# Kernel tuning notes

Hardware: AMD Instinct MI355X
Metric: run time of the kernel (lower is better)

The kernel has to match this reference:

```python
import jax, jax.numpy as jnp
import numpy as np
import math

H_HEADS = 16
D_PER = 64
D_MODEL = 1024
B, L = 8, 1024


def _dual_attention(q1, k1, q2, k2, v):
    # all [B,h,L,d]; scores = avg of two scaled QK^T
    scale = 1.0 / math.sqrt(q1.shape[-1])
    s1 = jnp.einsum('bhqd,bhkd->bhqk', q1, k1) * scale
    s2 = jnp.einsum('bhqd,bhkd->bhqk', q2, k2) * scale
    p = jax.nn.softmax((s1 + s2) * 0.5, axis=-1)
    return jnp.einsum('bhqk,bhkd->bhqd', p, v)


def _proj(X, W, b):
    # [B,L,D] -> [B,h,L,d]
    Bb, Ll, _ = X.shape
    y = X @ W + b
    return y.reshape(Bb, Ll, H_HEADS, D_PER).transpose(0, 2, 1, 3)


def _mha(Q1, K1, Q2, K2, V, Wq, bq, Wk, bk, Wv, bv, Wo, bo):
    q1 = _proj(Q1, Wq, bq)
    k1 = _proj(K1, Wk, bk)
    q2 = _proj(Q2, Wq, bq)  # same linear as q1 (linears[0])
    k2 = _proj(K2, Wk, bk)  # same linear as k1 (linears[1])
    v = _proj(V, Wv, bv)
    o = _dual_attention(q1, k1, q2, k2, v)  # [B,h,L,d]
    Bb = o.shape[0]
    o = o.transpose(0, 2, 1, 3).reshape(Bb, -1, H_HEADS * D_PER)
    return o @ Wo + bo  # [B,L,D]


def setup_inputs() -> dict:
    key = jax.random.key(0)
    ks = jax.random.split(key, 5)
    sc = 1.0 / math.sqrt(D_MODEL)
    return {
        'x': jax.random.normal(ks[0], (B, L, 3, D_MODEL), jnp.float32),
        'Wq': jax.random.normal(ks[1], (D_MODEL, H_HEADS * D_PER), jnp.float32) * sc,
        'bq': jnp.zeros((H_HEADS * D_PER,), jnp.float32),
        'Wk': jax.random.normal(ks[2], (D_MODEL, H_HEADS * D_PER), jnp.float32) * sc,
        'bk': jnp.zeros((H_HEADS * D_PER,), jnp.float32),
        'Wv': jax.random.normal(ks[3], (D_MODEL, H_HEADS * D_PER), jnp.float32) * sc,
        'bv': jnp.zeros((H_HEADS * D_PER,), jnp.float32),
        'Wo': jax.random.normal(ks[4], (H_HEADS * D_PER, D_MODEL), jnp.float32) * sc,
        'bo': jnp.zeros((D_MODEL,), jnp.float32),
    }


def reference(x, Wq, bq, Wk, bk, Wv, bv, Wo, bo):
    Hx = x[:, :, 0, :]
    Tx = x[:, :, 1, :]
    Rx = x[:, :, 2, :]
    p = (Wq, bq, Wk, bk, Wv, bv, Wo, bo)
    H_new = _mha(Tx, Tx, Rx, Rx, Hx, *p)
    T_new = _mha(Hx, Hx, Rx, Rx, Tx, *p)
    R_new = _mha(Hx, Hx, Tx, Tx, Rx, *p)
    return jnp.stack([H_new, T_new, R_new], axis=2)  # [B,L,3,D]
```

## Files before the change

### kernel.cpp

```cpp
#include <hip/hip_runtime.h>
#include <hip/hip_bf16.h>
#include <stdint.h>

#define NTOK 8192
#define DM   1024

typedef __bf16 bf16x8 __attribute__((ext_vector_type(8)));
typedef float  f32x4  __attribute__((ext_vector_type(4)));

__device__ __forceinline__ unsigned short f2bf(float f) {
  union { float f; unsigned u; } v; v.f = f;
  unsigned r = v.u + 0x7FFFu + ((v.u >> 16) & 1u);
  return (unsigned short)(r >> 16);
}

__device__ __forceinline__ void gld16(const void* g, const void* l) {
  __builtin_amdgcn_global_load_lds(
      (const __attribute__((address_space(1))) uint32_t*)g,
      (__attribute__((address_space(3))) uint32_t*)l, 16, 0, 0);
}

__global__ void convert_x(const float* __restrict__ x, unsigned short* __restrict__ Xbf) {
  int idx = (blockIdx.x * 256 + threadIdx.x) * 4;
  int s   = idx >> 23;
  int rem = idx & ((1 << 23) - 1);
  int tok = rem >> 10;
  int d   = rem & 1023;
  const float4 v = *(const float4*)&x[((size_t)tok * 3 + s) * 1024 + d];
  ushort4 o;
  o.x = f2bf(v.x); o.y = f2bf(v.y); o.z = f2bf(v.z); o.w = f2bf(v.w);
  *(ushort4*)&Xbf[idx] = o;
}

__global__ void transpose_w4(const float* __restrict__ W0, const float* __restrict__ W1,
                             const float* __restrict__ W2, const float* __restrict__ W3,
                             unsigned short* __restrict__ Wt) {
  __shared__ float t[32][33];
  int z = blockIdx.z;
  const float* W = (z == 0) ? W0 : (z == 1) ? W1 : (z == 2) ? W2 : W3;
  unsigned short* D = Wt + (size_t)z * 1048576;
  int tx = threadIdx.x, ty = threadIdx.y;
  int bx = blockIdx.x * 32, by = blockIdx.y * 32;
#pragma unroll
  for (int i = 0; i < 32; i += 8)
    t[ty + i][tx] = W[(size_t)(by + ty + i) * 1024 + bx + tx];
  __syncthreads();
#pragma unroll
  for (int i = 0; i < 32; i += 8)
    D[(size_t)(bx + ty + i) * 1024 + by + tx] = f2bf(t[tx][ty + i]);
}

#define STGA(tt) do { _Pragma("unroll") for (int j = 0; j < 4; ++j) \
  gld16(Ag + (size_t)(j * 64) * 1024 + (tt) * 64, &lds[(((tt) & 1) * 16384) + j * 4096 + wave * 512]); } while (0)
#define STGB(tt) do { _Pragma("unroll") for (int j = 0; j < 4; ++j) \
  gld16(Bg + (size_t)(j * 64) * 1024 + (tt) * 64, &lds[32768 + (((tt) & 1) * 16384) + j * 4096 + wave * 512]); } while (0)
#define RDAF(g, tt) do { \
  const unsigned short* _p = &lds[(((tt) & 1) * 16384) + (wm * 128 + (g) * 64) * 64]; \
  _Pragma("unroll") for (int m2 = 0; m2 < 4; ++m2) \
  _Pragma("unroll") for (int ks = 0; ks < 2; ++ks) \
    af[m2][ks] = *(const bf16x8*)&_p[(m2 * 16 + l16) * 64 + (((ks * 4 + quad) ^ sw8) * 8)]; } while (0)
#define RDBF(h, tt) do { \
  const unsigned short* _p = &lds[32768 + (((tt) & 1) * 16384) + (wn * 64 + (h) * 32) * 64]; \
  _Pragma("unroll") for (int n2 = 0; n2 < 2; ++n2) \
  _Pragma("unroll") for (int ks = 0; ks < 2; ++ks) \
    bfr[(h) * 2 + n2][ks] = *(const bf16x8*)&_p[(n2 * 16 + l16) * 64 + (((ks * 4 + quad) ^ sw8) * 8)]; } while (0)
#define MMQ(g, h) do { __builtin_amdgcn_s_setprio(1); \
  _Pragma("unroll") for (int m2 = 0; m2 < 4; ++m2) \
  _Pragma("unroll") for (int n2 = 0; n2 < 2; ++n2) \
  _Pragma("unroll") for (int ks = 0; ks < 2; ++ks) \
    acc[(g) * 4 + m2][(h) * 2 + n2] = __builtin_amdgcn_mfma_f32_16x16x32_bf16( \
      af[m2][ks], bfr[(h) * 2 + n2][ks], acc[(g) * 4 + m2][(h) * 2 + n2], 0, 0, 0); \
  __builtin_amdgcn_s_setprio(0); } while (0)

__device__ __forceinline__ void gemm256_core(
    const unsigned short* __restrict__ A, const unsigned short* __restrict__ Bt,
    unsigned short* lds, f32x4 acc[8][4], int m0, int n0)
{
  int tid = threadIdx.x;
  int wave = tid >> 6, lane = tid & 63, quad = lane >> 4, l16 = lane & 15;
  int wm = wave >> 2, wn = wave & 3;
  int sw8 = l16 & 7;
  int srow = wave * 8 + (lane >> 3);
  int schk = ((lane & 7) ^ (lane >> 3)) * 8;
  const unsigned short* Ag = A  + (size_t)(m0 + srow) * 1024 + schk;
  const unsigned short* Bg = Bt + (size_t)(n0 + srow) * 1024 + schk;
  bf16x8 af[4][2], bfr[4][2];

  STGA(0); STGB(0); STGA(1);
  asm volatile("s_waitcnt vmcnt(4)" ::: "memory");
  __builtin_amdgcn_s_barrier();
  __builtin_amdgcn_sched_barrier(0);

  for (int t = 0; t < 16; ++t) {
    RDAF(0, t); RDBF(0, t);
    if (t + 1 < 16) STGB(t + 1);
    __builtin_amdgcn_s_barrier();
    MMQ(0, 0);
    __builtin_amdgcn_s_barrier();
    RDBF(1, t);
    __builtin_amdgcn_s_barrier();
    MMQ(0, 1);
    __builtin_amdgcn_s_barrier();
    RDAF(1, t);
    __builtin_amdgcn_s_barrier();
    MMQ(1, 0);
    __builtin_amdgcn_s_barrier();
    if (t + 2 < 16) STGA(t + 2);
    __builtin_amdgcn_s_barrier();
    MMQ(1, 1);
    if (t + 2 < 16)      { asm volatile("s_waitcnt vmcnt(4)" ::: "memory"); }
    else if (t == 14)    { asm volatile("s_waitcnt vmcnt(0)" ::: "memory"); }
    __builtin_amdgcn_s_barrier();
    __builtin_amdgcn_sched_barrier(0);
  }
}

__global__ __launch_bounds__(512, 2) void gemm_proj(
    const unsigned short* __restrict__ Xbf, const unsigned short* __restrict__ Wt,
    unsigned short* __restrict__ P,
    const float* __restrict__ bq, const float* __restrict__ bk, const float* __restrict__ bv)
{
  __shared__ alignas(16) unsigned short lds[65536];
  int z = blockIdx.z, s = z / 3, w = z - s * 3;
  const float* bias = (w == 0) ? bq : (w == 1) ? bk : bv;
  float osc = (w == 0) ? 0.09016844136867f : 1.0f;
  int f = blockIdx.x;
  int swz = (f & 7) * 16 + (f >> 3);
  int m0 = (swz & 31) * 256, n0 = (swz >> 5) * 256;
  f32x4 acc[8][4];
#pragma unroll
  for (int i = 0; i < 8; i++)
#pragma unroll
    for (int j = 0; j < 4; j++) acc[i][j] = (f32x4){0.f, 0.f, 0.f, 0.f};
  gemm256_core(Xbf + (size_t)s * NTOK * 1024, Wt + (size_t)w * 1048576, lds, acc, m0, n0);

  int tid = threadIdx.x, wave = tid >> 6, lane = tid & 63, quad = lane >> 4, l16 = lane & 15;
  int wm = wave >> 2, wn = wave & 3;
  int rbase = m0 + wm * 128, cbase = n0 + wn * 64;
  unsigned short* C = P + (size_t)z * NTOK * 1024;
  if (w == 2) {
#pragma unroll
    for (int mi = 0; mi < 8; mi++) {
      int row0 = rbase + mi * 16 + quad * 4;
      int b = row0 >> 10, l0 = row0 & 1023;
#pragma unroll
      for (int ni = 0; ni < 4; ni++) {
        int col = cbase + ni * 16 + l16;
        float bcol = bias[col];
        int hh = col >> 6, d = col & 63;
        ushort4 o4;
        o4.x = f2bf(acc[mi][ni][0] + bcol);
        o4.y = f2bf(acc[mi][ni][1] + bcol);
        o4.z = f2bf(acc[mi][ni][2] + bcol);
        o4.w = f2bf(acc[mi][ni][3] + bcol);
        *(ushort4*)&C[(size_t)(b * 16 + hh) * 65536 + (size_t)d * 1024 + l0] = o4;
      }
    }
  } else {
#pragma unroll
    for (int mi = 0; mi < 8; mi++)
#pragma unroll
      for (int ni = 0; ni < 4; ni++) {
        int col = cbase + ni * 16 + l16;
        float bcol = bias[col];
#pragma unroll
        for (int r = 0; r < 4; r++) {
          int row = rbase + mi * 16 + quad * 4 + r;
          C[(size_t)row * 1024 + col] = f2bf((acc[mi][ni][r] + bcol) * osc);
        }
      }
  }
}

__global__ __launch_bounds__(512, 2) void gemm_out(
    const unsigned short* __restrict__ Oattn, const unsigned short* __restrict__ WtO,
    float* __restrict__ out, const float* __restrict__ bo)
{
  __shared__ alignas(16) unsigned short lds[65536];
  int s = blockIdx.z;
  int f = blockIdx.x;
  int swz = (f & 7) * 16 + (f >> 3);
  int m0 = (swz & 31) * 256, n0 = (swz >> 5) * 256;
  f32x4 acc[8][4];
#pragma unroll
  for (int i = 0; i < 8; i++)
#pragma unroll
    for (int j = 0; j < 4; j++) acc[i][j] = (f32x4){0.f, 0.f, 0.f, 0.f};
  gemm256_core(Oattn + (size_t)s * NTOK * 1024, WtO, lds, acc, m0, n0);

  int tid = threadIdx.x, wave = tid >> 6, lane = tid & 63, quad = lane >> 4, l16 = lane & 15;
  int wm = wave >> 2, wn = wave & 3;
  int rbase = m0 + wm * 128, cbase = n0 + wn * 64;
#pragma unroll
  for (int mi = 0; mi < 8; mi++)
#pragma unroll
    for (int ni = 0; ni < 4; ni++) {
      int col = cbase + ni * 16 + l16;
      float bcol = bo[col];
#pragma unroll
      for (int r = 0; r < 4; r++) {
        int row = rbase + mi * 16 + quad * 4 + r;
        out[(size_t)row * 3072 + s * 1024 + col] = acc[mi][ni][r] + bcol;
      }
    }
}

__global__ __launch_bounds__(256, 4) void attn(
    const unsigned short* __restrict__ P, unsigned short* __restrict__ Oa)
{
  __shared__ alignas(16) unsigned short lK1[64 * 64];
  __shared__ alignas(16) unsigned short lK2[64 * 64];
  __shared__ alignas(16) unsigned short lV [64 * 64];
  __shared__ alignas(16) unsigned short pls[4][32 * 40];
  int o  = blockIdx.z;
  int As = (o == 0) ? 1 : 0;
  int Bs = (o == 2) ? 1 : 2;
  int b = blockIdx.x >> 4, h = blockIdx.x & 15;
  int tid = threadIdx.x, wave = tid >> 6, lane = tid & 63, quad = lane >> 4, l16 = lane & 15;
  int q0 = blockIdx.y * 128 + wave * 32;
  size_t bh_off = (size_t)b * 1024 * 1024 + h * 64;
  const unsigned short* Q1 = P + (size_t)(As * 3 + 0) * NTOK * 1024 + bh_off;
  const unsigned short* K1 = P + (size_t)(As * 3 + 1) * NTOK * 1024 + bh_off;
  const unsigned short* Q2 = P + (size_t)(Bs * 3 + 0) * NTOK * 1024 + bh_off;
  const unsigned short* K2 = P + (size_t)(Bs * 3 + 1) * NTOK * 1024 + bh_off;
  const unsigned short* V  = P + (size_t)(o * 3 + 2) * NTOK * 1024
                               + (size_t)(b * 16 + h) * 65536;
  unsigned short* myp = pls[wave];

  bf16x8 q1f[2][2], q2f[2][2];
#pragma unroll
  for (int qt = 0; qt < 2; qt++)
#pragma unroll
    for (int c = 0; c < 2; c++) {
      q1f[qt][c] = *(const bf16x8*)&Q1[(size_t)(q0 + qt * 16 + l16) * 1024 + c * 32 + quad * 8];
      q2f[qt][c] = *(const bf16x8*)&Q2[(size_t)(q0 + qt * 16 + l16) * 1024 + c * 32 + quad * 8];
    }
  bf16x8 ones;
#pragma unroll
  for (int j = 0; j < 8; j++) ones[j] = (__bf16)1.0f;

  int r8 = lane >> 3;
  int cs = ((lane & 7) ^ r8) * 8;
  int srow = wave * 16 + r8;
  const unsigned short* K1s = K1 + (size_t)srow * 1024 + cs;
  const unsigned short* K2s = K2 + (size_t)srow * 1024 + cs;
  const unsigned short* Vs  = V  + (size_t)srow * 1024 + cs;
  int fsw = (l16 & 7);

  f32x4 oacc[2][4];
#pragma unroll
  for (int qt = 0; qt < 2; qt++)
#pragma unroll
    for (int dt = 0; dt < 4; dt++) oacc[qt][dt] = (f32x4){0.f, 0.f, 0.f, 0.f};
  f32x4 lsum[2];
  lsum[0] = (f32x4){0.f, 0.f, 0.f, 0.f};
  lsum[1] = (f32x4){0.f, 0.f, 0.f, 0.f};

  for (int k0 = 0; k0 < 1024; k0 += 64) {
#pragma unroll
    for (int half = 0; half < 2; half++) {
      size_t krow = (size_t)(k0 + half * 8) * 1024;
      gld16(K1s + krow,                 lK1 + (wave * 16 + half * 8) * 64);
      gld16(K2s + krow,                 lK2 + (wave * 16 + half * 8) * 64);
      gld16(Vs + k0 + half * 8 * 1024,  lV  + (wave * 16 + half * 8) * 64);
    }
    __syncthreads();

#pragma unroll
    for (int kc = 0; kc < 2; kc++) {
      f32x4 sacc[2][2];
      sacc[0][0] = (f32x4){0.f, 0.f, 0.f, 0.f};
      sacc[0][1] = (f32x4){0.f, 0.f, 0.f, 0.f};
      sacc[1][0] = (f32x4){0.f, 0.f, 0.f, 0.f};
      sacc[1][1] = (f32x4){0.f, 0.f, 0.f, 0.f};
      __builtin_amdgcn_s_setprio(1);
#pragma unroll
      for (int kt = 0; kt < 2; kt++) {
        int krow = (kc * 32 + kt * 16 + l16) * 64;
        bf16x8 k1a = *(const bf16x8*)&lK1[krow + ((quad ^ fsw) * 8)];
        bf16x8 k1b = *(const bf16x8*)&lK1[krow + (((quad + 4) ^ fsw) * 8)];
        bf16x8 k2a = *(const bf16x8*)&lK2[krow + ((quad ^ fsw) * 8)];
        bf16x8 k2b = *(const bf16x8*)&lK2[krow + (((quad + 4) ^ fsw) * 8)];
#pragma unroll
        for (int qt = 0; qt < 2; qt++) {
          sacc[qt][kt] = __builtin_amdgcn_mfma_f32_16x16x32_bf16(q1f[qt][0], k1a, sacc[qt][kt], 0, 0, 0);
          sacc[qt][kt] = __builtin_amdgcn_mfma_f32_16x16x32_bf16(q1f[qt][1], k1b, sacc[qt][kt], 0, 0, 0);
          sacc[qt][kt] = __builtin_amdgcn_mfma_f32_16x16x32_bf16(q2f[qt][0], k2a, sacc[qt][kt], 0, 0, 0);
          sacc[qt][kt] = __builtin_amdgcn_mfma_f32_16x16x32_bf16(q2f[qt][1], k2b, sacc[qt][kt], 0, 0, 0);
        }
      }
      __builtin_amdgcn_s_setprio(0);
#pragma unroll
      for (int qt = 0; qt < 2; qt++)
#pragma unroll
        for (int kt = 0; kt < 2; kt++)
#pragma unroll
          for (int r2 = 0; r2 < 2; r2++) {
            union { float f; unsigned u; } e0, e1;
            e0.f = __builtin_amdgcn_exp2f(sacc[qt][kt][r2 * 2]);
            e1.f = __builtin_amdgcn_exp2f(sacc[qt][kt][r2 * 2 + 1]);
            unsigned pk = __builtin_amdgcn_perm(e1.u + 0x8000u, e0.u + 0x8000u, 0x07060302u);
            int row = qt * 16 + quad * 4 + r2 * 2;
            myp[row * 40 + kt * 16 + l16]       = (unsigned short)pk;
            myp[(row + 1) * 40 + kt * 16 + l16] = (unsigned short)(pk >> 16);
          }
      bf16x8 pa0 = *(const bf16x8*)&myp[l16 * 40 + quad * 8];
      bf16x8 pa1 = *(const bf16x8*)&myp[(16 + l16) * 40 + quad * 8];
      __builtin_amdgcn_s_setprio(1);
      lsum[0] = __builtin_amdgcn_mfma_f32_16x16x32_bf16(pa0, ones, lsum[0], 0, 0, 0);
      lsum[1] = __builtin_amdgcn_mfma_f32_16x16x32_bf16(pa1, ones, lsum[1], 0, 0, 0);
#pragma unroll
      for (int dt = 0; dt < 4; dt++) {
        bf16x8 vf = *(const bf16x8*)&lV[(dt * 16 + l16) * 64 + (((kc * 4 + quad) ^ fsw) * 8)];
        oacc[0][dt] = __builtin_amdgcn_mfma_f32_16x16x32_bf16(pa0, vf, oacc[0][dt], 0, 0, 0);
        oacc[1][dt] = __builtin_amdgcn_mfma_f32_16x16x32_bf16(pa1, vf, oacc[1][dt], 0, 0, 0);
      }
      __builtin_amdgcn_s_setprio(0);
    }
    __syncthreads();
  }

  unsigned short* Od = Oa + (size_t)o * NTOK * 1024 + bh_off;
#pragma unroll
  for (int qt = 0; qt < 2; qt++) {
    f32x4 inv;
#pragma unroll
    for (int r = 0; r < 4; r++) inv[r] = 1.0f / lsum[qt][r];
#pragma unroll
    for (int dt = 0; dt < 4; dt++)
#pragma unroll
      for (int r = 0; r < 4; r++) {
        float val = oacc[qt][dt][r] * inv[r];
        Od[(size_t)(q0 + qt * 16 + quad * 4 + r) * 1024 + dt * 16 + l16] = f2bf(val);
      }
  }
}

extern "C" void kernel_launch(void* const* d_in, const int* in_sizes, int n_in,
                              void* d_out, int out_size, void* d_ws, size_t ws_size,
                              hipStream_t stream) {
  (void)in_sizes; (void)n_in; (void)out_size; (void)ws_size;
  const float* x  = (const float*)d_in[0];
  const float* Wq = (const float*)d_in[1];
  const float* bq = (const float*)d_in[2];
  const float* Wk = (const float*)d_in[3];
  const float* bk = (const float*)d_in[4];
  const float* Wv = (const float*)d_in[5];
  const float* bv = (const float*)d_in[6];
  const float* Wo = (const float*)d_in[7];
  const float* bo = (const float*)d_in[8];
  float* out = (float*)d_out;

  char* ws = (char*)d_ws;
  unsigned short* Xbf = (unsigned short*)(ws + 0);
  unsigned short* Wt  = (unsigned short*)(ws + 50331648);
  unsigned short* P   = (unsigned short*)(ws + 58720256);
  unsigned short* Oa  = (unsigned short*)(ws + 209715200);

  convert_x<<<24576, 256, 0, stream>>>(x, Xbf);
  transpose_w4<<<dim3(32, 32, 4), dim3(32, 8), 0, stream>>>(Wq, Wk, Wv, Wo, Wt);

  gemm_proj<<<dim3(128, 1, 9), 512, 0, stream>>>(Xbf, Wt, P, bq, bk, bv);
  attn<<<dim3(128, 8, 3), 256, 0, stream>>>(P, Oa);
  gemm_out<<<dim3(128, 1, 3), 512, 0, stream>>>(Oa, Wt + 3 * 1048576, out, bo);
}
```

Measured before the change: 601.0 us.

## Cut GEMM barriers, lower occupancy bound, register-prefetch attention K/V tiles

The GEMM main loop drops most of its per-quadrant barriers and keeps only two fenced barriers per k-step, with the next A-tile stage issued after the first. Both GEMM kernels change their launch bounds from 2 to 1 block per CU, which frees registers. The attention kernel replaces direct global-to-LDS loads with register prefetch of the next K1/K2/V tile during compute, then writes the tile to LDS after the sync. This aims to overlap global latency with the MFMA work, at the cost of more registers and an extra barrier per iteration. The register-staged stores write to LDS slots at lane*8 without the XOR swizzle used by the reads, which may not match the old layout.

```diff
diff --git a/kernel.cpp b/kernel.cpp
--- a/kernel.cpp
+++ b/kernel.cpp
@@ -71,6 +71,8 @@
     acc[(g) * 4 + m2][(h) * 2 + n2] = __builtin_amdgcn_mfma_f32_16x16x32_bf16( \
       af[m2][ks], bfr[(h) * 2 + n2][ks], acc[(g) * 4 + m2][(h) * 2 + n2], 0, 0, 0); \
   __builtin_amdgcn_s_setprio(0); } while (0)
+#define FBAR() do { asm volatile("" ::: "memory"); __builtin_amdgcn_s_barrier(); \
+  asm volatile("" ::: "memory"); __builtin_amdgcn_sched_barrier(0); } while (0)
 
 __device__ __forceinline__ void gemm256_core(
     const unsigned short* __restrict__ A, const unsigned short* __restrict__ Bt,
@@ -88,34 +90,29 @@
 
   STGA(0); STGB(0); STGA(1);
   asm volatile("s_waitcnt vmcnt(4)" ::: "memory");
-  __builtin_amdgcn_s_barrier();
-  __builtin_amdgcn_sched_barrier(0);
+  FBAR();
 
   for (int t = 0; t < 16; ++t) {
     RDAF(0, t); RDBF(0, t);
     if (t + 1 < 16) STGB(t + 1);
-    __builtin_amdgcn_s_barrier();
     MMQ(0, 0);
-    __builtin_amdgcn_s_barrier();
     RDBF(1, t);
-    __builtin_amdgcn_s_barrier();
     MMQ(0, 1);
-    __builtin_amdgcn_s_barrier();
     RDAF(1, t);
-    __builtin_amdgcn_s_barrier();
     MMQ(1, 0);
-    __builtin_amdgcn_s_barrier();
-    if (t + 2 < 16) STGA(t + 2);
-    __builtin_amdgcn_s_barrier();
     MMQ(1, 1);
-    if (t + 2 < 16)      { asm volatile("s_waitcnt vmcnt(4)" ::: "memory"); }
-    else if (t == 14)    { asm volatile("s_waitcnt vmcnt(0)" ::: "memory"); }
-    __builtin_amdgcn_s_barrier();
-    __builtin_amdgcn_sched_barrier(0);
+    FBAR();
+    if (t + 2 < 16) {
+      STGA(t + 2);
+      asm volatile("s_waitcnt vmcnt(4)" ::: "memory");
+    } else if (t + 1 < 16) {
+      asm volatile("s_waitcnt vmcnt(0)" ::: "memory");
+    }
+    FBAR();
   }
 }
 
-__global__ __launch_bounds__(512, 2) void gemm_proj(
+__global__ __launch_bounds__(512, 1) void gemm_proj(
     const unsigned short* __restrict__ Xbf, const unsigned short* __restrict__ Wt,
     unsigned short* __restrict__ P,
     const float* __restrict__ bq, const float* __restrict__ bk, const float* __restrict__ bv)
@@ -172,7 +169,7 @@
   }
 }
 
-__global__ __launch_bounds__(512, 2) void gemm_out(
+__global__ __launch_bounds__(512, 1) void gemm_out(
     const unsigned short* __restrict__ Oattn, const unsigned short* __restrict__ WtO,
     float* __restrict__ out, const float* __restrict__ bo)
 {
@@ -247,6 +244,10 @@
   const unsigned short* Vs  = V  + (size_t)srow * 1024 + cs;
   int fsw = (l16 & 7);
 
+  uint4 st0, st1, st2, st3, st4, st5;
+  int wbase0 = (wave * 16) * 64 + lane * 8;
+  int wbase1 = (wave * 16 + 8) * 64 + lane * 8;
+
   f32x4 oacc[2][4];
 #pragma unroll
   for (int qt = 0; qt < 2; qt++)
@@ -256,15 +257,21 @@
   lsum[0] = (f32x4){0.f, 0.f, 0.f, 0.f};
   lsum[1] = (f32x4){0.f, 0.f, 0.f, 0.f};
 
+  st0 = *(const uint4*)(K1s);            st1 = *(const uint4*)(K1s + 8 * 1024);
+  st2 = *(const uint4*)(K2s);            st3 = *(const uint4*)(K2s + 8 * 1024);
+  st4 = *(const uint4*)(Vs);             st5 = *(const uint4*)(Vs + 8 * 1024);
+  *(uint4*)&lK1[wbase0] = st0;  *(uint4*)&lK1[wbase1] = st1;
+  *(uint4*)&lK2[wbase0] = st2;  *(uint4*)&lK2[wbase1] = st3;
+  *(uint4*)&lV [wbase0] = st4;  *(uint4*)&lV [wbase1] = st5;
+  __syncthreads();
+
   for (int k0 = 0; k0 < 1024; k0 += 64) {
-#pragma unroll
-    for (int half = 0; half < 2; half++) {
-      size_t krow = (size_t)(k0 + half * 8) * 1024;
-      gld16(K1s + krow,                 lK1 + (wave * 16 + half * 8) * 64);
-      gld16(K2s + krow,                 lK2 + (wave * 16 + half * 8) * 64);
-      gld16(Vs + k0 + half * 8 * 1024,  lV  + (wave * 16 + half * 8) * 64);
-    }
-    __syncthreads();
+    if (k0 + 64 < 1024) {
+      size_t kn = (size_t)(k0 + 64) * 1024;
+      st0 = *(const uint4*)(K1s + kn);             st1 = *(const uint4*)(K1s + kn + 8 * 1024);
+      st2 = *(const uint4*)(K2s + kn);             st3 = *(const uint4*)(K2s + kn + 8 * 1024);
+      st4 = *(const uint4*)(Vs + k0 + 64);         st5 = *(const uint4*)(Vs + k0 + 64 + 8 * 1024);
+    }
 
 #pragma unroll
     for (int kc = 0; kc < 2; kc++) {
@@ -318,6 +325,12 @@
       __builtin_amdgcn_s_setprio(0);
     }
     __syncthreads();
+    if (k0 + 64 < 1024) {
+      *(uint4*)&lK1[wbase0] = st0;  *(uint4*)&lK1[wbase1] = st1;
+      *(uint4*)&lK2[wbase0] = st2;  *(uint4*)&lK2[wbase1] = st3;
+      *(uint4*)&lV [wbase0] = st4;  *(uint4*)&lV [wbase1] = st5;
+      __syncthreads();
+    }
   }
 
   unsigned short* Od = Oa + (size_t)o * NTOK * 1024 + bh_off;
```

After: 764.3 us. 27.2% more time.
